# Optimization experiments

Hardware: AMD Instinct MI355X
Metric: run time of the kernel (lower is better)

## Reference

```python
import jax, jax.numpy as jnp
import numpy as np

B, H, W = 8, 64, 64
DIM, HEADS, WS = 512, 8, 8
C2 = DIM // 2            # attention branch channels
HD = C2 // HEADS         # head dim = 32
NH, NW = H // WS, W // WS
WIN = WS * WS            # tokens per window = 64
SCALE = HD ** -0.5
EPS = 1e-5


def layer_norm(x, g, b):
    m = jnp.mean(x, axis=-1, keepdims=True)
    v = jnp.mean((x - m) ** 2, axis=-1, keepdims=True)
    return (x - m) * jax.lax.rsqrt(v + EPS) * g + b


def dwconv3x3(x, w, b=None):
    # x: (N, C, h, w); w: (C, 1, 3, 3) depthwise
    out = jax.lax.conv_general_dilated(
        x, w, window_strides=(1, 1), padding='SAME',
        feature_group_count=x.shape[1],
        dimension_numbers=('NCHW', 'OIHW', 'NCHW'))
    if b is not None:
        out = out + b[None, :, None, None]
    return out


def setup_inputs() -> dict:
    key = jax.random.key(0)
    ks = jax.random.split(key, 8)
    r = lambda k, s: (jax.random.normal(k, s, jnp.float32) * 0.02)
    return {
        'x': jax.random.normal(ks[0], (B, H * W, DIM), jnp.float32),
        'norm1_g': jnp.ones((DIM,), jnp.float32),
        'norm1_b': jnp.zeros((DIM,), jnp.float32),
        'qkv_w': r(ks[1], (C2, 3 * C2)),
        'qkv_b': jnp.zeros((3 * C2,), jnp.float32),
        'lepe_w': r(ks[2], (C2, 1, 3, 3)),
        'lepe_b': jnp.zeros((C2,), jnp.float32),
        'convloc_w': r(ks[3], (C2, 1, 3, 3)),
        'proj_w': r(ks[4], (DIM, DIM)),
        'proj_b': jnp.zeros((DIM,), jnp.float32),
        'norm2_g': jnp.ones((DIM,), jnp.float32),
        'norm2_b': jnp.zeros((DIM,), jnp.float32),
        'fc1_w': r(ks[5], (DIM, 4 * DIM)),
        'fc1_b': jnp.zeros((4 * DIM,), jnp.float32),
        'fc2_w': r(ks[6], (4 * DIM, DIM)),
        'fc2_b': jnp.zeros((DIM,), jnp.float32),
    }


def reference(x, norm1_g, norm1_b, qkv_w, qkv_b, lepe_w, lepe_b, convloc_w,
              proj_w, proj_b, norm2_g, norm2_b, fc1_w, fc1_b, fc2_w, fc2_b):
    img = layer_norm(x, norm1_g, norm1_b)                      # (B, L, DIM)

    # qkv from first half of channels
    qkv = img[..., :C2] @ qkv_w + qkv_b                        # (B, L, 3*C2)
    qkv = qkv.reshape(B, H * W, 3, C2)
    q, k, v = qkv[:, :, 0], qkv[:, :, 1], qkv[:, :, 2]

    def win6(t):  # (B, L, C2) -> (B, NH, NW, WS, WS, C2)
        return t.reshape(B, NH, WS, NW, WS, C2).transpose(0, 1, 3, 2, 4, 5)

    def to_heads(t6):
        return t6.reshape(-1, WIN, HEADS, HD).transpose(0, 2, 1, 3)

    qh = to_heads(win6(q)) * SCALE
    kh = to_heads(win6(k))

    # v + LePE: depthwise 3x3 conv applied per-window
    vw = win6(v).transpose(0, 1, 2, 5, 3, 4).reshape(-1, C2, WS, WS)
    lepe = dwconv3x3(vw, lepe_w, lepe_b)                       # (nWin, C2, WS, WS)
    vh = vw.reshape(-1, HEADS, HD, WIN).transpose(0, 1, 3, 2)
    leh = lepe.reshape(-1, HEADS, HD, WIN).transpose(0, 1, 3, 2)

    attn = jax.nn.softmax(jnp.einsum('nhqd,nhkd->nhqk', qh, kh), axis=-1)
    o = jnp.einsum('nhqk,nhkd->nhqd', attn, vh) + leh

    # merge windows back to (B, L, C2)
    o = o.transpose(0, 2, 1, 3).reshape(B, NH, NW, WS, WS, C2)
    o = o.transpose(0, 1, 3, 2, 4, 5).reshape(B, H * W, C2)

    # parallel depthwise-conv branch on second half of channels (no bias)
    x2 = img[..., C2:].transpose(0, 2, 1).reshape(B, C2, H, W)
    x2 = dwconv3x3(x2, convloc_w)
    x2 = x2.reshape(B, C2, H * W).transpose(0, 2, 1)

    local = jnp.concatenate([o, x2], axis=-1) @ proj_w + proj_b
    x = x + local

    # MLP_FFN: Linear -> GELU -> Linear
    h = jax.nn.gelu(layer_norm(x, norm2_g, norm2_b) @ fc1_w + fc1_b,
                    approximate=False)
    x = x + (h @ fc2_w + fc2_b)
    return x
```

## Files before the change

kernel.cpp:

```cpp
#include <hip/hip_runtime.h>
#include <cstdint>
#include <cstddef>

typedef unsigned short u16;
typedef __attribute__((ext_vector_type(8))) short short8;
typedef __attribute__((ext_vector_type(4))) float f32x4;

#define DIM 512
#define C2  256
#define HD  32
#define SCALE_Q 0.17677669529663689f

__device__ __forceinline__ float bf2f(u16 u){ return __uint_as_float(((unsigned)u) << 16); }
__device__ __forceinline__ u16 f2bf(float f){
  unsigned u = __float_as_uint(f);
  unsigned r = (u + 0x7FFFu + ((u >> 16) & 1u)) >> 16;
  return (u16)r;
}

__device__ __forceinline__ f32x4 mfma16(short8 a, short8 b, f32x4 c){
  return __builtin_amdgcn_mfma_f32_16x16x32_bf16(a, b, c, 0, 0, 0);
}

__device__ __forceinline__ void gload16(const u16* g, u16* l){
  __builtin_amdgcn_global_load_lds((const __attribute__((address_space(1))) void*)g,
                                   (__attribute__((address_space(3))) void*)l, 16, 0, 0);
}

__device__ __forceinline__ float gelu_f(float v){
  float e = __expf(-1.702f * v);
  return v * __builtin_amdgcn_rcpf(1.0f + e);
}

__global__ __launch_bounds__(256) void transpose_kernel(const float* __restrict__ W,
                                                        u16* __restrict__ WT, int K, int N){
  __shared__ u16 Tl[32][33];
  int n0 = blockIdx.x * 32, k0 = blockIdx.y * 32;
  int tx = threadIdx.x & 31, ty = threadIdx.x >> 5;
#pragma unroll
  for (int i = 0; i < 4; i++){
    int k = ty * 4 + i;
    Tl[k][tx] = f2bf(W[(size_t)(k0 + k) * N + n0 + tx]);
  }
  __syncthreads();
#pragma unroll
  for (int i = 0; i < 4; i++){
    int n = ty * 4 + i;
    WT[(size_t)(n0 + n) * K + k0 + tx] = Tl[tx][n];
  }
}

__global__ __launch_bounds__(256) void ln_kernel(const float* __restrict__ x, const float* __restrict__ g,
                                                 const float* __restrict__ bta, u16* __restrict__ out){
  int row  = blockIdx.x * 4 + (threadIdx.x >> 6);
  int lane = threadIdx.x & 63;
  size_t base = (size_t)row * DIM + lane * 8;
  float4 v0 = *(const float4*)(x + base);
  float4 v1 = *(const float4*)(x + base + 4);
  float f[8] = {v0.x, v0.y, v0.z, v0.w, v1.x, v1.y, v1.z, v1.w};
  float s = 0.f;
#pragma unroll
  for (int j = 0; j < 8; j++) s += f[j];
#pragma unroll
  for (int m = 1; m < 64; m <<= 1) s += __shfl_xor(s, m, 64);
  float mean = s * (1.0f / DIM);
  float vs = 0.f;
#pragma unroll
  for (int j = 0; j < 8; j++){ float d = f[j] - mean; vs += d * d; }
#pragma unroll
  for (int m = 1; m < 64; m <<= 1) vs += __shfl_xor(vs, m, 64);
  float rstd = rsqrtf(vs * (1.0f / DIM) + 1e-5f);
  float4 g0 = *(const float4*)(g + lane * 8);
  float4 g1 = *(const float4*)(g + lane * 8 + 4);
  float4 b0 = *(const float4*)(bta + lane * 8);
  float4 b1 = *(const float4*)(bta + lane * 8 + 4);
  float gg[8] = {g0.x, g0.y, g0.z, g0.w, g1.x, g1.y, g1.z, g1.w};
  float bb[8] = {b0.x, b0.y, b0.z, b0.w, b1.x, b1.y, b1.z, b1.w};
  short8 o;
#pragma unroll
  for (int j = 0; j < 8; j++){
    float r = (f[j] - mean) * rstd * gg[j] + bb[j];
    o[j] = (short)f2bf(r);
  }
  *(short8*)(out + base) = o;
}

template<int EPI, bool OUT_BF16>
__global__ __launch_bounds__(512, 2) void gemm8_kernel(
    const u16* __restrict__ A, int lda,
    const u16* __restrict__ WT,
    const float* __restrict__ bias,
    const float* R, int ldr,
    void* Cv, int ldc, int K)
{
  __shared__ u16 Al[2][2][256 * 32];
  __shared__ u16 Bl[2][2][256 * 32];
  const int tid = threadIdx.x;
  const int l   = tid & 63;
  const int w   = tid >> 6;
  const int wr  = w >> 2;
  const int wc  = w & 3;
  const int l16 = l & 15, lhi = l >> 4;

  const int gx = gridDim.x;
  int bid = blockIdx.y * gx + blockIdx.x;
  int nwg = gx * gridDim.y;
  int sw  = (nwg & 7) ? bid : ((bid & 7) * (nwg >> 3) + (bid >> 3));
  const int col0 = (sw % gx) * 256, row0 = (sw / gx) * 256;
  const int NT = K >> 6;

  const int srow = w * 16 + (l >> 2);
  const int cs   = (((l & 3) ^ ((l >> 3) & 3)) * 8);
  const u16* pA = A  + (size_t)(row0 + srow) * lda + cs;
  const u16* pB = WT + (size_t)(col0 + srow) * K  + cs;
  const size_t a128 = (size_t)128 * lda, b128 = (size_t)128 * K;

  auto stageA = [&](int tt, int hh){
    if (tt < NT){
      size_t go = (size_t)tt * 64 + (size_t)hh * 32;
      gload16(pA + go,        &Al[tt & 1][hh][(w * 16) * 32]);
      gload16(pA + a128 + go, &Al[tt & 1][hh][(128 + w * 16) * 32]);
    }
  };
  auto stageB = [&](int tt, int hh){
    if (tt < NT){
      size_t go = (size_t)tt * 64 + (size_t)hh * 32;
      gload16(pB + go,        &Bl[tt & 1][hh][(w * 16) * 32]);
      gload16(pB + b128 + go, &Bl[tt & 1][hh][(128 + w * 16) * 32]);
    }
  };

  const int rdo = l16 * 32 + (lhi ^ ((l16 >> 1) & 3)) * 8;

  f32x4 acc[8][4] = {};
  short8 af[4], bf[4];

  stageA(0, 0); stageB(0, 0); stageA(0, 1); stageB(0, 1);
  stageA(1, 0); stageB(1, 0); stageA(1, 1); stageB(1, 1);
  asm volatile("s_waitcnt vmcnt(8)" ::: "memory");
  __builtin_amdgcn_sched_barrier(0);
  __builtin_amdgcn_s_barrier();

#define PHASE(BC, KH, QM, STAGES) do{                                                   \
    if ((QM) == 0){                                                                     \
      _Pragma("unroll")                                                                 \
      for (int n = 0; n < 4; n++)                                                       \
        bf[n] = *(const short8*)&Bl[BC][KH][(wc * 64 + n * 16) * 32 + rdo];             \
    }                                                                                   \
    _Pragma("unroll")                                                                   \
    for (int m = 0; m < 4; m++)                                                         \
      af[m] = *(const short8*)&Al[BC][KH][(wr * 128 + (QM) * 64 + m * 16) * 32 + rdo];  \
    STAGES;                                                                             \
    __builtin_amdgcn_s_barrier();                                                       \
    asm volatile("s_waitcnt lgkmcnt(0)" ::: "memory");                                  \
    __builtin_amdgcn_sched_barrier(0);                                                  \
    __builtin_amdgcn_s_setprio(1);                                                      \
    _Pragma("unroll")                                                                   \
    for (int m = 0; m < 4; m++)                                                         \
      _Pragma("unroll")                                                                 \
      for (int n = 0; n < 4; n++)                                                       \
        acc[(QM) * 4 + m][n] = mfma16(bf[n], af[m], acc[(QM) * 4 + m][n]);              \
    __builtin_amdgcn_s_setprio(0);                                                      \
    __builtin_amdgcn_s_barrier();                                                       \
  }while(0)

  for (int t = 0; t < NT; t++){
    const int bc = t & 1;
    PHASE(bc, 0, 0, (void)0);
    PHASE(bc, 0, 1, stageB(t + 2, 0));
    PHASE(bc, 1, 0, stageA(t + 2, 0));
    PHASE(bc, 1, 1, stageB(t + 2, 1));
    stageA(t + 2, 1);
    if (t + 2 < NT) asm volatile("s_waitcnt vmcnt(8)" ::: "memory");
    else            asm volatile("s_waitcnt vmcnt(0)" ::: "memory");
    __builtin_amdgcn_sched_barrier(0);
    __builtin_amdgcn_s_barrier();
  }
#undef PHASE

  float4 bvs[4];
#pragma unroll
  for (int n = 0; n < 4; n++)
    bvs[n] = *(const float4*)&bias[col0 + wc * 64 + n * 16 + lhi * 4];
#pragma unroll
  for (int mq = 0; mq < 8; mq++){
    int grow = row0 + wr * 128 + mq * 16 + l16;
#pragma unroll
    for (int n = 0; n < 4; n++){
      int gcol = col0 + wc * 64 + n * 16 + lhi * 4;
      float4 vv = { acc[mq][n][0] + bvs[n].x, acc[mq][n][1] + bvs[n].y,
                    acc[mq][n][2] + bvs[n].z, acc[mq][n][3] + bvs[n].w };
      if constexpr (EPI == 1){
        float4 rv = *(const float4*)&R[(size_t)grow * ldr + gcol];
        vv.x += rv.x; vv.y += rv.y; vv.z += rv.z; vv.w += rv.w;
      }
      if constexpr (EPI == 2){
        vv.x = gelu_f(vv.x); vv.y = gelu_f(vv.y); vv.z = gelu_f(vv.z); vv.w = gelu_f(vv.w);
      }
      if constexpr (OUT_BF16){
        ushort4 o4 = { f2bf(vv.x), f2bf(vv.y), f2bf(vv.z), f2bf(vv.w) };
        *(ushort4*)&((u16*)Cv)[(size_t)grow * ldc + gcol] = o4;
      } else {
        *(float4*)&((float*)Cv)[(size_t)grow * ldc + gcol] = vv;
      }
    }
  }
}

__global__ __launch_bounds__(64) void attn_kernel(
    const u16* __restrict__ qkv, const float* __restrict__ lw,
    const float* __restrict__ lb, u16* __restrict__ out)
{
  __shared__ float Ks[64][33];
  __shared__ float Vs[64][33];
  __shared__ float Wle[32][9];
  __shared__ float Lb[32];
  int head = blockIdx.x & 7, win = blockIdx.x >> 3;
  int wx = win & 7, wy = (win >> 3) & 7, b = win >> 6;
  int l  = threadIdx.x;
  int py = l >> 3, px = l & 7;
  size_t t = (size_t)b * 4096 + (size_t)(wy * 8 + py) * 64 + (wx * 8 + px);
  const u16* base = qkv + t * 768 + head * HD;

  float q[32];
#pragma unroll
  for (int j = 0; j < 32; j += 8){
    short8 vq = *(const short8*)(base + j);
    short8 vk = *(const short8*)(base + 256 + j);
    short8 vv = *(const short8*)(base + 512 + j);
#pragma unroll
    for (int e = 0; e < 8; e++){
      q[j + e]     = bf2f((u16)vq[e]) * SCALE_Q;
      Ks[l][j + e] = bf2f((u16)vk[e]);
      Vs[l][j + e] = bf2f((u16)vv[e]);
    }
  }
  for (int i = l; i < 288; i += 64) Wle[i / 9][i % 9] = lw[(head * 32 + i / 9) * 9 + (i % 9)];
  if (l < 32) Lb[l] = lb[head * 32 + l];
  __syncthreads();

  float sc[64];
  float mx = -1e30f;
#pragma unroll
  for (int k = 0; k < 64; k++){
    float s = 0.f;
#pragma unroll
    for (int d = 0; d < 32; d++) s += q[d] * Ks[k][d];
    sc[k] = s; mx = fmaxf(mx, s);
  }
  float sum = 0.f;
#pragma unroll
  for (int k = 0; k < 64; k++){ float e = __expf(sc[k] - mx); sc[k] = e; sum += e; }
  float inv = 1.0f / sum;
  float o[32];
#pragma unroll
  for (int d = 0; d < 32; d++) o[d] = 0.f;
#pragma unroll
  for (int k = 0; k < 64; k++){
    float p = sc[k] * inv;
#pragma unroll
    for (int d = 0; d < 32; d++) o[d] += p * Vs[k][d];
  }
#pragma unroll
  for (int ky = 0; ky < 3; ky++){
    int yy = py + ky - 1;
    if (yy < 0 || yy >= 8) continue;
#pragma unroll
    for (int kx = 0; kx < 3; kx++){
      int xx = px + kx - 1;
      if (xx < 0 || xx >= 8) continue;
      int kp = yy * 8 + xx;
#pragma unroll
      for (int d = 0; d < 32; d++) o[d] += Wle[d][ky * 3 + kx] * Vs[kp][d];
    }
  }
  u16* op = out + t * DIM + head * HD;
#pragma unroll
  for (int d = 0; d < 32; d += 4){
    ushort4 o4 = { f2bf(o[d] + Lb[d]), f2bf(o[d + 1] + Lb[d + 1]),
                   f2bf(o[d + 2] + Lb[d + 2]), f2bf(o[d + 3] + Lb[d + 3]) };
    *(ushort4*)&op[d] = o4;
  }
}

__global__ __launch_bounds__(256) void convloc_kernel(const u16* __restrict__ img,
    const float* __restrict__ w, u16* __restrict__ out){
  int c  = threadIdx.x;
  int pg = blockIdx.x;
  int b  = pg >> 8;
  int p0 = (pg & 255) * 16;
  float wt[9];
#pragma unroll
  for (int i = 0; i < 9; i++) wt[i] = w[c * 9 + i];
  for (int pi = 0; pi < 16; pi++){
    int p = p0 + pi;
    int y = p >> 6, x = p & 63;
    float acc = 0.f;
#pragma unroll
    for (int ky = 0; ky < 3; ky++){
      int yy = y + ky - 1;
      if (yy < 0 || yy >= 64) continue;
#pragma unroll
      for (int kx = 0; kx < 3; kx++){
        int xx = x + kx - 1;
        if (xx < 0 || xx >= 64) continue;
        acc += wt[ky * 3 + kx] * bf2f(img[((size_t)b * 4096 + yy * 64 + xx) * DIM + C2 + c]);
      }
    }
    out[((size_t)b * 4096 + p) * DIM + C2 + c] = f2bf(acc);
  }
}

extern "C" void kernel_launch(void* const* d_in, const int* in_sizes, int n_in,
                              void* d_out, int out_size, void* d_ws, size_t ws_size,
                              hipStream_t stream){
  const float* x      = (const float*)d_in[0];
  const float* n1g    = (const float*)d_in[1];
  const float* n1b    = (const float*)d_in[2];
  const float* qkv_w  = (const float*)d_in[3];
  const float* qkv_b  = (const float*)d_in[4];
  const float* lepe_w = (const float*)d_in[5];
  const float* lepe_b = (const float*)d_in[6];
  const float* conv_w = (const float*)d_in[7];
  const float* proj_w = (const float*)d_in[8];
  const float* proj_b = (const float*)d_in[9];
  const float* n2g    = (const float*)d_in[10];
  const float* n2b    = (const float*)d_in[11];
  const float* fc1_w  = (const float*)d_in[12];
  const float* fc1_b  = (const float*)d_in[13];
  const float* fc2_w  = (const float*)d_in[14];
  const float* fc2_b  = (const float*)d_in[15];
  float* out = (float*)d_out;

  char* ws = (char*)d_ws;
  u16* img     = (u16*)(ws + 0);
  u16* qkvb    = (u16*)(ws + 33554432ull);
  u16* localb  = (u16*)(ws + 83886080ull);
  u16* y       = (u16*)(ws + 0);
  u16* h       = (u16*)(ws + 33554432ull);
  u16* qkv_wT  = (u16*)(ws + 167772160ull);
  u16* proj_wT = (u16*)(ws + 167772160ull + 393216ull);
  u16* fc1_wT  = (u16*)(ws + 167772160ull + 393216ull + 524288ull);
  u16* fc2_wT  = (u16*)(ws + 167772160ull + 393216ull + 524288ull + 2097152ull);
  float* xa    = (float*)d_out;

  { dim3 g(24, 8);  transpose_kernel<<<g, 256, 0, stream>>>(qkv_w,  qkv_wT,  256, 768);  }
  { dim3 g(16, 16); transpose_kernel<<<g, 256, 0, stream>>>(proj_w, proj_wT, 512, 512);  }
  { dim3 g(64, 16); transpose_kernel<<<g, 256, 0, stream>>>(fc1_w,  fc1_wT,  512, 2048); }
  { dim3 g(16, 64); transpose_kernel<<<g, 256, 0, stream>>>(fc2_w,  fc2_wT,  2048, 512); }

  ln_kernel<<<8192, 256, 0, stream>>>(x, n1g, n1b, img);

  dim3 gq(3, 128);
  gemm8_kernel<0, true><<<gq, 512, 0, stream>>>(img, DIM, qkv_wT, qkv_b, nullptr, 0, qkvb, 768, 256);

  attn_kernel<<<4096, 64, 0, stream>>>(qkvb, lepe_w, lepe_b, localb);
  convloc_kernel<<<2048, 256, 0, stream>>>(img, conv_w, localb);

  dim3 gp(2, 128);
  gemm8_kernel<1, false><<<gp, 512, 0, stream>>>(localb, DIM, proj_wT, proj_b, x, DIM, xa, DIM, 512);

  ln_kernel<<<8192, 256, 0, stream>>>(xa, n2g, n2b, y);

  dim3 g1(8, 128);
  gemm8_kernel<2, true><<<g1, 512, 0, stream>>>(y, DIM, fc1_wT, fc1_b, nullptr, 0, h, 2048, 512);

  dim3 g2(2, 128);
  gemm8_kernel<1, false><<<g2, 512, 0, stream>>>(h, 2048, fc2_wT, fc2_b, xa, DIM, out, DIM, 2048);
}
```

Baseline: 444.6 us.

## Vectorize convloc, merge weight transposes, and repad attention shared memory

Rewrites the depthwise local conv so each thread handles four channels with vector loads and weights staged in shared memory, instead of scalar per-channel loads over a 16-pixel loop. Merges the four weight-transpose launches into one kernel to cut launch overhead. Changes attention shared-memory padding and wraps GEMM template instances in named kernels. Repadding to 36 may introduce bank conflicts for strided column access.

```diff
diff --git a/kernel.cpp b/kernel.cpp
--- a/kernel.cpp
+++ b/kernel.cpp
@@ -32,10 +32,19 @@
   return v * __builtin_amdgcn_rcpf(1.0f + e);
 }
 
-__global__ __launch_bounds__(256) void transpose_kernel(const float* __restrict__ W,
-                                                        u16* __restrict__ WT, int K, int N){
+__global__ __launch_bounds__(256) void transpose_all_kernel(
+    const float* __restrict__ qkv_w, const float* __restrict__ proj_w,
+    const float* __restrict__ fc1_w, const float* __restrict__ fc2_w,
+    u16* __restrict__ qkv_wT, u16* __restrict__ proj_wT,
+    u16* __restrict__ fc1_wT, u16* __restrict__ fc2_wT){
   __shared__ u16 Tl[32][33];
-  int n0 = blockIdx.x * 32, k0 = blockIdx.y * 32;
+  int b = blockIdx.x;
+  const float* W; u16* WT; int K, N, nx, ti;
+  if (b < 192)      { W = qkv_w;  WT = qkv_wT;  K = 256;  N = 768;  nx = 24; ti = b; }
+  else if (b < 448) { W = proj_w; WT = proj_wT; K = 512;  N = 512;  nx = 16; ti = b - 192; }
+  else if (b < 1472){ W = fc1_w;  WT = fc1_wT;  K = 512;  N = 2048; nx = 64; ti = b - 448; }
+  else              { W = fc2_w;  WT = fc2_wT;  K = 2048; N = 512;  nx = 16; ti = b - 1472; }
+  int n0 = (ti % nx) * 32, k0 = (ti / nx) * 32;
   int tx = threadIdx.x & 31, ty = threadIdx.x >> 5;
 #pragma unroll
   for (int i = 0; i < 4; i++){
@@ -86,7 +95,7 @@
 }
 
 template<int EPI, bool OUT_BF16>
-__global__ __launch_bounds__(512, 2) void gemm8_kernel(
+__device__ __forceinline__ void gemm8_body(
     const u16* __restrict__ A, int lda,
     const u16* __restrict__ WT,
     const float* __restrict__ bias,
@@ -207,12 +216,29 @@
   }
 }
 
+__global__ __launch_bounds__(512, 2) void gemm_qkv_kernel(const u16* A, int lda, const u16* WT,
+    const float* bias, const float* R, int ldr, void* Cv, int ldc, int K){
+  gemm8_body<0, true>(A, lda, WT, bias, R, ldr, Cv, ldc, K);
+}
+__global__ __launch_bounds__(512, 2) void gemm_proj_kernel(const u16* A, int lda, const u16* WT,
+    const float* bias, const float* R, int ldr, void* Cv, int ldc, int K){
+  gemm8_body<1, false>(A, lda, WT, bias, R, ldr, Cv, ldc, K);
+}
+__global__ __launch_bounds__(512, 2) void gemm_fc1_kernel(const u16* A, int lda, const u16* WT,
+    const float* bias, const float* R, int ldr, void* Cv, int ldc, int K){
+  gemm8_body<2, true>(A, lda, WT, bias, R, ldr, Cv, ldc, K);
+}
+__global__ __launch_bounds__(512, 2) void gemm_fc2_kernel(const u16* A, int lda, const u16* WT,
+    const float* bias, const float* R, int ldr, void* Cv, int ldc, int K){
+  gemm8_body<1, false>(A, lda, WT, bias, R, ldr, Cv, ldc, K);
+}
+
 __global__ __launch_bounds__(64) void attn_kernel(
     const u16* __restrict__ qkv, const float* __restrict__ lw,
     const float* __restrict__ lb, u16* __restrict__ out)
 {
-  __shared__ float Ks[64][33];
-  __shared__ float Vs[64][33];
+  __shared__ float Ks[64][36];
+  __shared__ float Vs[64][36];
   __shared__ float Wle[32][9];
   __shared__ float Lb[32];
   int head = blockIdx.x & 7, win = blockIdx.x >> 3;
@@ -285,30 +311,36 @@
 
 __global__ __launch_bounds__(256) void convloc_kernel(const u16* __restrict__ img,
     const float* __restrict__ w, u16* __restrict__ out){
-  int c  = threadIdx.x;
-  int pg = blockIdx.x;
-  int b  = pg >> 8;
-  int p0 = (pg & 255) * 16;
-  float wt[9];
-#pragma unroll
-  for (int i = 0; i < 9; i++) wt[i] = w[c * 9 + i];
-  for (int pi = 0; pi < 16; pi++){
-    int p = p0 + pi;
-    int y = p >> 6, x = p & 63;
-    float acc = 0.f;
-#pragma unroll
-    for (int ky = 0; ky < 3; ky++){
-      int yy = y + ky - 1;
-      if (yy < 0 || yy >= 64) continue;
-#pragma unroll
-      for (int kx = 0; kx < 3; kx++){
-        int xx = x + kx - 1;
-        if (xx < 0 || xx >= 64) continue;
-        acc += wt[ky * 3 + kx] * bf2f(img[((size_t)b * 4096 + yy * 64 + xx) * DIM + C2 + c]);
-      }
-    }
-    out[((size_t)b * 4096 + p) * DIM + C2 + c] = f2bf(acc);
-  }
+  __shared__ float Wl[9 * 256];
+  int tid = threadIdx.x;
+  for (int i = tid; i < 2304; i += 256){
+    int ch = i / 9, tp = i - ch * 9;
+    Wl[tp * 256 + ch] = w[i];
+  }
+  __syncthreads();
+  int c  = (tid & 63) * 4;
+  int pq = tid >> 6;
+  int p  = blockIdx.x * 4 + pq;
+  int b  = p >> 12;
+  int pi = p & 4095;
+  int y = pi >> 6, x = pi & 63;
+  float a0 = 0.f, a1 = 0.f, a2 = 0.f, a3 = 0.f;
+#pragma unroll
+  for (int ky = 0; ky < 3; ky++){
+    int yy = y + ky - 1;
+    if (yy < 0 || yy >= 64) continue;
+#pragma unroll
+    for (int kx = 0; kx < 3; kx++){
+      int xx = x + kx - 1;
+      if (xx < 0 || xx >= 64) continue;
+      ushort4 v = *(const ushort4*)&img[((size_t)b * 4096 + yy * 64 + xx) * DIM + C2 + c];
+      float4 wv = *(const float4*)&Wl[(ky * 3 + kx) * 256 + c];
+      a0 += wv.x * bf2f(v.x); a1 += wv.y * bf2f(v.y);
+      a2 += wv.z * bf2f(v.z); a3 += wv.w * bf2f(v.w);
+    }
+  }
+  ushort4 o4 = { f2bf(a0), f2bf(a1), f2bf(a2), f2bf(a3) };
+  *(ushort4*)&out[((size_t)b * 4096 + pi) * DIM + C2 + c] = o4;
 }
 
 extern "C" void kernel_launch(void* const* d_in, const int* in_sizes, int n_in,
@@ -344,27 +376,25 @@
   u16* fc2_wT  = (u16*)(ws + 167772160ull + 393216ull + 524288ull + 2097152ull);
   float* xa    = (float*)d_out;
 
-  { dim3 g(24, 8);  transpose_kernel<<<g, 256, 0, stream>>>(qkv_w,  qkv_wT,  256, 768);  }
-  { dim3 g(16, 16); transpose_kernel<<<g, 256, 0, stream>>>(proj_w, proj_wT, 512, 512);  }
-  { dim3 g(64, 16); transpose_kernel<<<g, 256, 0, stream>>>(fc1_w,  fc1_wT,  512, 2048); }
-  { dim3 g(16, 64); transpose_kernel<<<g, 256, 0, stream>>>(fc2_w,  fc2_wT,  2048, 512); }
+  transpose_all_kernel<<<2496, 256, 0, stream>>>(qkv_w, proj_w, fc1_w, fc2_w,
+                                                 qkv_wT, proj_wT, fc1_wT, fc2_wT);
 
   ln_kernel<<<8192, 256, 0, stream>>>(x, n1g, n1b, img);
 
   dim3 gq(3, 128);
-  gemm8_kernel<0, true><<<gq, 512, 0, stream>>>(img, DIM, qkv_wT, qkv_b, nullptr, 0, qkvb, 768, 256);
+  gemm_qkv_kernel<<<gq, 512, 0, stream>>>(img, DIM, qkv_wT, qkv_b, nullptr, 0, qkvb, 768, 256);
 
   attn_kernel<<<4096, 64, 0, stream>>>(qkvb, lepe_w, lepe_b, localb);
-  convloc_kernel<<<2048, 256, 0, stream>>>(img, conv_w, localb);
+  convloc_kernel<<<8192, 256, 0, stream>>>(img, conv_w, localb);
 
   dim3 gp(2, 128);
-  gemm8_kernel<1, false><<<gp, 512, 0, stream>>>(localb, DIM, proj_wT, proj_b, x, DIM, xa, DIM, 512);
+  gemm_proj_kernel<<<gp, 512, 0, stream>>>(localb, DIM, proj_wT, proj_b, x, DIM, xa, DIM, 512);
 
   ln_kernel<<<8192, 256, 0, stream>>>(xa, n2g, n2b, y);
 
   dim3 g1(8, 128);
-  gemm8_kernel<2, true><<<g1, 512, 0, stream>>>(y, DIM, fc1_wT, fc1_b, nullptr, 0, h, 2048, 512);
+  gemm_fc1_kernel<<<g1, 512, 0, stream>>>(y, DIM, fc1_wT, fc1_b, nullptr, 0, h, 2048, 512);
 
   dim3 g2(2, 128);
-  gemm8_kernel<1, false><<<g2, 512, 0, stream>>>(h, 2048, fc2_wT, fc2_b, xa, DIM, out, DIM, 2048);
-}
+  gemm_fc2_kernel<<<g2, 512, 0, stream>>>(h, 2048, fc2_wT, fc2_b, xa, DIM, out, DIM, 2048);
+}
```

Measured after the change: 408.9 us. 1.09x faster.
